# Kernel optimization log

Measured on AMD Instinct MI355X. Metric: run time of the kernel, lower is better.

The kernel has to match this reference:

```python
import jax, jax.numpy as jnp
import numpy as np

N_SRC, N_DST, E = 10000, 40000, 1_280_000
IN_DIM, OUT_DIM, FEAT, O_DIM = 128, 64, 64, 300


def setup_inputs() -> dict:
    key = jax.random.key(0)
    ks = jax.random.split(key, 10)
    s = 0.05
    return {
        "h": jax.random.normal(ks[0], (N_SRC, IN_DIM), jnp.float32),
        "o": jax.random.normal(ks[1], (N_DST, O_DIM), jnp.float32),
        "tfidf": jax.random.normal(ks[2], (E, FEAT), jnp.float32),
        "W_fc": jax.random.normal(ks[3], (IN_DIM, OUT_DIM), jnp.float32) * s,
        "W_fc1": jax.random.normal(ks[4], (O_DIM, OUT_DIM), jnp.float32) * s,
        "W_feat": jax.random.normal(ks[5], (FEAT, OUT_DIM), jnp.float32) * s,
        "b_feat": jax.random.normal(ks[6], (OUT_DIM,), jnp.float32) * s,
        "W_attn": jax.random.normal(ks[7], (OUT_DIM, 1), jnp.float32) * s,
        "edge_src": jax.random.randint(ks[8], (E,), 0, N_SRC, jnp.int32),
        "edge_dst": jax.random.randint(ks[9], (E,), 0, N_DST, jnp.int32),
    }


def reference(h, o, tfidf, W_fc, W_fc1, W_feat, b_feat, W_attn, edge_src, edge_dst):
    n_dst = o.shape[0]
    # node projections: z on sentence (src) nodes via fc, on word (dst) nodes via fc1
    z_src = h @ W_fc                      # [N_SRC, D]
    z_dst = o @ W_fc1                     # [N_DST, D]
    # edge attention: z2 = src.z + dst.z + feat_fc(tfidfembed)
    dfeat = tfidf @ W_feat + b_feat       # [E, D]
    z2 = z_src[edge_src] + z_dst[edge_dst] + dfeat
    z3 = jnp.where(z2 > 0, z2, 0.01 * z2)  # leaky_relu, torch default slope
    e = (z3 @ W_attn)[:, 0]               # [E]
    # segment softmax over incoming edges of each dst (word) node
    m = jax.ops.segment_max(e, edge_dst, num_segments=n_dst)   # [N_DST]
    e_exp = jnp.exp(e - m[edge_dst])                           # [E]
    denom = jax.ops.segment_sum(e_exp, edge_dst, num_segments=n_dst)
    alpha = e_exp / jnp.maximum(denom, 1e-9)[edge_dst]         # [E]
    # weighted sum of src z into dst mailbox
    out = jax.ops.segment_sum(alpha[:, None] * z_src[edge_src], edge_dst,
                              num_segments=n_dst)              # [N_DST, D]
    return out
```

## Files before the change

### kernel.cpp

```cpp
#include <hip/hip_runtime.h>
#include <hip/hip_bf16.h>

#define N_SRC 10000
#define N_DST 40000
#define NE    1280000
#define IN_DIM 128
#define O_DIM  300
#define D      64
#define FEAT   64
#define NB     157

typedef __bf16 bf16x8 __attribute__((ext_vector_type(8)));
typedef __bf16 bf16x4 __attribute__((ext_vector_type(4)));
typedef float  f32x4  __attribute__((ext_vector_type(4)));

__global__ __launch_bounds__(256) void k_zsrc(const float* __restrict__ h,
                                              const float* __restrict__ Wfc,
                                              float* __restrict__ z,
                                              __bf16* __restrict__ zh){
    __shared__ float w[IN_DIM * D];
    for (int i = threadIdx.x; i < IN_DIM * D; i += blockDim.x) w[i] = Wfc[i];
    __syncthreads();
    int lane = threadIdx.x & 63;
    int wid  = blockIdx.x * 4 + (threadIdx.x >> 6);
    int nw   = gridDim.x * 4;
    for (int row = wid; row < N_SRC; row += nw){
        const f32x4* hp = (const f32x4*)(h + (size_t)row * IN_DIM);
        float acc = 0.f;
        #pragma unroll 4
        for (int k4 = 0; k4 < IN_DIM / 4; ++k4){
            f32x4 hv = hp[k4];
            int k = k4 * 4;
            acc += hv[0] * w[(k + 0) * D + lane];
            acc += hv[1] * w[(k + 1) * D + lane];
            acc += hv[2] * w[(k + 2) * D + lane];
            acc += hv[3] * w[(k + 3) * D + lane];
        }
        z[(size_t)row * D + lane]  = acc;
        zh[(size_t)row * D + lane] = (__bf16)acc;
    }
}

__global__ __launch_bounds__(256) void k_zdst(const float* __restrict__ o,
                                              const float* __restrict__ Wfc1,
                                              float* __restrict__ z){
    extern __shared__ float w[];
    for (int i = threadIdx.x; i < O_DIM * D; i += blockDim.x) w[i] = Wfc1[i];
    __syncthreads();
    int lane = threadIdx.x & 63;
    int wid  = blockIdx.x * 4 + (threadIdx.x >> 6);
    int nw   = gridDim.x * 4;
    for (int row = wid; row < N_DST; row += nw){
        const f32x4* op = (const f32x4*)(o + (size_t)row * O_DIM);
        float acc = 0.f;
        #pragma unroll 5
        for (int k4 = 0; k4 < O_DIM / 4; ++k4){
            f32x4 ov = op[k4];
            int k = k4 * 4;
            acc += ov[0] * w[(k + 0) * D + lane];
            acc += ov[1] * w[(k + 1) * D + lane];
            acc += ov[2] * w[(k + 2) * D + lane];
            acc += ov[3] * w[(k + 3) * D + lane];
        }
        z[(size_t)row * D + lane] = acc;
    }
}

__global__ __launch_bounds__(256) void k_hist(const int* __restrict__ edst,
                                              int* __restrict__ cnt){
    int i = blockIdx.x * blockDim.x + threadIdx.x;
    if (i < NE) atomicAdd(&cnt[edst[i]], 1);
}

__device__ __forceinline__ int block_incl_scan(int c, int* wsum){
    int lane = threadIdx.x & 63, w = threadIdx.x >> 6;
    int v = c;
    #pragma unroll
    for (int off = 1; off < 64; off <<= 1){
        int u = __shfl_up(v, off);
        if (lane >= off) v += u;
    }
    if (lane == 63) wsum[w] = v;
    __syncthreads();
    int add = 0;
    for (int ww = 0; ww < w; ++ww) add += wsum[ww];
    return v + add;
}

__global__ __launch_bounds__(256) void k_scan1(const int* __restrict__ cnt,
                                               int* __restrict__ bsum){
    __shared__ int wsum[4];
    int i = blockIdx.x * 256 + threadIdx.x;
    int c = (i < N_DST) ? cnt[i] : 0;
    int lane = threadIdx.x & 63, w = threadIdx.x >> 6;
    int v = c;
    #pragma unroll
    for (int off = 1; off < 64; off <<= 1) v += __shfl_xor(v, off);
    if (lane == 0) wsum[w] = v;
    __syncthreads();
    if (threadIdx.x == 0)
        bsum[blockIdx.x] = wsum[0] + wsum[1] + wsum[2] + wsum[3];
}

__global__ __launch_bounds__(256) void k_scan2(int* __restrict__ bsum){
    __shared__ int wsum[4];
    int i = threadIdx.x;
    int c = (i < NB) ? bsum[i] : 0;
    int v = block_incl_scan(c, wsum);
    if (i < NB) bsum[i] = v - c;
}

__global__ __launch_bounds__(256) void k_scan3(const int* __restrict__ cnt,
                                               const int* __restrict__ bsum,
                                               int* __restrict__ csr,
                                               int* __restrict__ cursor){
    __shared__ int wsum[4];
    int i = blockIdx.x * 256 + threadIdx.x;
    int c = (i < N_DST) ? cnt[i] : 0;
    int v = block_incl_scan(c, wsum);
    int val = bsum[blockIdx.x] + v - c;
    if (i < N_DST){ csr[i] = val; cursor[i] = val; }
    if (blockIdx.x == 0 && threadIdx.x == 0) csr[N_DST] = NE;
}

__global__ __launch_bounds__(256) void k_bucket(const int* __restrict__ esrc,
                                                const int* __restrict__ edst,
                                                int* __restrict__ cursor,
                                                int* __restrict__ ssrc,
                                                int* __restrict__ sdst,
                                                int* __restrict__ sedge){
    int e = blockIdx.x * blockDim.x + threadIdx.x;
    if (e >= NE) return;
    int d = edst[e];
    int pos = atomicAdd(&cursor[d], 1);
    ssrc[pos]  = esrc[e];
    sdst[pos]  = d;
    sedge[pos] = e;
}

__global__ __launch_bounds__(256) void k_edge(
        const float* __restrict__ tfidf,
        const int*   __restrict__ ssrc, const int* __restrict__ sdst,
        const int*   __restrict__ sedge,
        const __bf16* __restrict__ zsrch, const float* __restrict__ zdst,
        const float* __restrict__ Wfeat, const float* __restrict__ bfeat,
        const float* __restrict__ Wattn,
        float* __restrict__ escore_p){
    int lane = threadIdx.x & 63;
    int lo = lane & 15, g = lane >> 4;

    bf16x8 afr[4][2];
    #pragma unroll
    for (int mt = 0; mt < 4; ++mt){
        int m = mt * 16 + lo;
        #pragma unroll
        for (int kh = 0; kh < 2; ++kh){
            #pragma unroll
            for (int j = 0; j < 8; ++j){
                int k = kh * 32 + g * 8 + j;
                afr[mt][kh][j] = (__bf16)Wfeat[k * D + m];
            }
        }
    }
    f32x4 bf4[4], wa4[4];
    #pragma unroll
    for (int mt = 0; mt < 4; ++mt){
        int db = mt * 16 + g * 4;
        bf4[mt] = *(const f32x4*)(bfeat + db);
        wa4[mt] = *(const f32x4*)(Wattn + db);
    }

    int wid = blockIdx.x * 4 + (threadIdx.x >> 6);
    int nw  = gridDim.x * 4;
    for (int tile = wid; tile < NE / 16; tile += nw){
        int p  = tile * 16 + lo;
        int se = sedge[p], ss = ssrc[p], sd = sdst[p];

        const float* trow = tfidf + (size_t)se * FEAT;
        bf16x8 bfr[2];
        #pragma unroll
        for (int kh = 0; kh < 2; ++kh){
            f32x4 fa = *(const f32x4*)(trow + kh * 32 + g * 8);
            f32x4 fb = *(const f32x4*)(trow + kh * 32 + g * 8 + 4);
            #pragma unroll
            for (int j = 0; j < 4; ++j){
                bfr[kh][j]     = (__bf16)fa[j];
                bfr[kh][4 + j] = (__bf16)fb[j];
            }
        }

        float pacc = 0.f;
        #pragma unroll
        for (int mt = 0; mt < 4; ++mt){
            f32x4 acc = {0.f, 0.f, 0.f, 0.f};
            acc = __builtin_amdgcn_mfma_f32_16x16x32_bf16(afr[mt][0], bfr[0], acc, 0, 0, 0);
            acc = __builtin_amdgcn_mfma_f32_16x16x32_bf16(afr[mt][1], bfr[1], acc, 0, 0, 0);
            int db = mt * 16 + g * 4;
            bf16x4 zs = *(const bf16x4*)(zsrch + (size_t)ss * D + db);
            f32x4  zd = *(const f32x4*)(zdst + (size_t)sd * D + db);
            #pragma unroll
            for (int r = 0; r < 4; ++r){
                float z2 = acc[r] + (float)zs[r] + zd[r] + bf4[mt][r];
                float z3 = z2 > 0.f ? z2 : 0.01f * z2;
                pacc += z3 * wa4[mt][r];
            }
        }
        pacc += __shfl_xor(pacc, 16);
        pacc += __shfl_xor(pacc, 32);
        if (lane < 16)
            escore_p[tile * 16 + lane] = pacc;
    }
}

__global__ __launch_bounds__(256) void k_post(const int* __restrict__ csr,
                                              const int* __restrict__ ssrc,
                                              const float* __restrict__ escore_p,
                                              const float* __restrict__ zsrc,
                                              float* __restrict__ out){
    int lane = threadIdx.x & 63;
    int d    = blockIdx.x * 4 + (threadIdx.x >> 6);
    if (d >= N_DST) return;
    int beg = csr[d], end = csr[d + 1];

    float m = -3.4e38f;
    for (int j = beg + lane; j < end; j += 64)
        m = fmaxf(m, escore_p[j]);
    #pragma unroll
    for (int off = 1; off < 64; off <<= 1)
        m = fmaxf(m, __shfl_xor(m, off));

    float ssum = 0.f;
    for (int j = beg + lane; j < end; j += 64)
        ssum += __expf(escore_p[j] - m);
    #pragma unroll
    for (int off = 1; off < 64; off <<= 1)
        ssum += __shfl_xor(ssum, off);
    float inv = 1.f / fmaxf(ssum, 1e-9f);

    float acc = 0.f;
    for (int base = beg; base < end; base += 64){
        int n = end - base; if (n > 64) n = 64;
        int   sj = 0;
        float aj = 0.f;
        if (base + lane < end){
            sj = ssrc[base + lane];
            aj = __expf(escore_p[base + lane] - m) * inv;
        }
        for (int t = 0; t < n; ++t){
            int   s = __shfl(sj, t);
            float a = __shfl(aj, t);
            acc += a * zsrc[(size_t)s * D + lane];
        }
    }
    out[(size_t)d * D + lane] = acc;
}

extern "C" void kernel_launch(void* const* d_in, const int* in_sizes, int n_in,
                              void* d_out, int out_size, void* d_ws, size_t ws_size,
                              hipStream_t stream) {
    const float* h     = (const float*)d_in[0];
    const float* o     = (const float*)d_in[1];
    const float* tfidf = (const float*)d_in[2];
    const float* Wfc   = (const float*)d_in[3];
    const float* Wfc1  = (const float*)d_in[4];
    const float* Wfeat = (const float*)d_in[5];
    const float* bfeat = (const float*)d_in[6];
    const float* Wattn = (const float*)d_in[7];
    const int*   esrc  = (const int*)d_in[8];
    const int*   edst  = (const int*)d_in[9];
    float* out = (float*)d_out;

    float*  ws      = (float*)d_ws;
    float*  zsrc    = ws;
    float*  zdst    = ws + 640000;
    __bf16* zsrch   = (__bf16*)(ws + 3200000);
    float*  escorep = ws + 3520000;
    int*    ssrc    = (int*)(ws + 4800000);
    int*    sdst    = (int*)(ws + 6080000);
    int*    sedge   = (int*)(ws + 7360000);
    int*    cnt     = (int*)(ws + 8640000);
    int*    csr     = (int*)(ws + 8680000);
    int*    cursor  = (int*)(ws + 8720002);
    int*    bsum    = (int*)(ws + 8760002);

    hipMemsetAsync(cnt, 0, N_DST * sizeof(int), stream);

    k_zsrc<<<256, 256, 0, stream>>>(h, Wfc, zsrc, zsrch);
    k_zdst<<<512, 256, O_DIM * D * sizeof(float), stream>>>(o, Wfc1, zdst);
    k_hist<<<NE / 256, 256, 0, stream>>>(edst, cnt);
    k_scan1<<<NB, 256, 0, stream>>>(cnt, bsum);
    k_scan2<<<1, 256, 0, stream>>>(bsum);
    k_scan3<<<NB, 256, 0, stream>>>(cnt, bsum, csr, cursor);
    k_bucket<<<NE / 256, 256, 0, stream>>>(esrc, edst, cursor, ssrc, sdst, sedge);
    k_edge<<<4096, 256, 0, stream>>>(tfidf, ssrc, sdst, sedge, zsrch, zdst,
                                     Wfeat, bfeat, Wattn, escorep);
    k_post<<<N_DST / 4, 256, 0, stream>>>(csr, ssrc, escorep, zsrc, out);
}
```

Measured before the change: 950.3 us.

## Replace bucket pass with atomic ranks and scatter scores from edge kernel

The histogram kernel now records each edge's atomic rank within its destination, and the separate bucket kernel is removed. The edge kernel reads tfidf rows, src and dst in original edge order, so the big tfidf read becomes coalesced instead of a random gather, and it scatters the score and src index to csr[dst]+rank. The projection kernels also compute four rows per wave so each shared-memory weight load is reused across rows. The cost is a scattered write of scores in the edge kernel and a nondeterministic within-segment order from the atomics.

```diff
diff --git a/kernel.cpp b/kernel.cpp
--- a/kernel.cpp
+++ b/kernel.cpp
@@ -24,20 +24,26 @@
     int lane = threadIdx.x & 63;
     int wid  = blockIdx.x * 4 + (threadIdx.x >> 6);
     int nw   = gridDim.x * 4;
-    for (int row = wid; row < N_SRC; row += nw){
-        const f32x4* hp = (const f32x4*)(h + (size_t)row * IN_DIM);
-        float acc = 0.f;
+    for (int r0 = wid * 4; r0 < N_SRC; r0 += nw * 4){
+        const f32x4* p0 = (const f32x4*)(h + (size_t)(r0 + 0) * IN_DIM);
+        const f32x4* p1 = (const f32x4*)(h + (size_t)(r0 + 1) * IN_DIM);
+        const f32x4* p2 = (const f32x4*)(h + (size_t)(r0 + 2) * IN_DIM);
+        const f32x4* p3 = (const f32x4*)(h + (size_t)(r0 + 3) * IN_DIM);
+        float a0 = 0.f, a1 = 0.f, a2 = 0.f, a3 = 0.f;
         #pragma unroll 4
         for (int k4 = 0; k4 < IN_DIM / 4; ++k4){
-            f32x4 hv = hp[k4];
-            int k = k4 * 4;
-            acc += hv[0] * w[(k + 0) * D + lane];
-            acc += hv[1] * w[(k + 1) * D + lane];
-            acc += hv[2] * w[(k + 2) * D + lane];
-            acc += hv[3] * w[(k + 3) * D + lane];
-        }
-        z[(size_t)row * D + lane]  = acc;
-        zh[(size_t)row * D + lane] = (__bf16)acc;
+            f32x4 v0 = p0[k4], v1 = p1[k4], v2 = p2[k4], v3 = p3[k4];
+            #pragma unroll
+            for (int i = 0; i < 4; ++i){
+                float wv = w[(k4 * 4 + i) * D + lane];
+                a0 += v0[i] * wv; a1 += v1[i] * wv;
+                a2 += v2[i] * wv; a3 += v3[i] * wv;
+            }
+        }
+        z[(size_t)(r0 + 0) * D + lane] = a0; zh[(size_t)(r0 + 0) * D + lane] = (__bf16)a0;
+        z[(size_t)(r0 + 1) * D + lane] = a1; zh[(size_t)(r0 + 1) * D + lane] = (__bf16)a1;
+        z[(size_t)(r0 + 2) * D + lane] = a2; zh[(size_t)(r0 + 2) * D + lane] = (__bf16)a2;
+        z[(size_t)(r0 + 3) * D + lane] = a3; zh[(size_t)(r0 + 3) * D + lane] = (__bf16)a3;
     }
 }
 
@@ -50,26 +56,34 @@
     int lane = threadIdx.x & 63;
     int wid  = blockIdx.x * 4 + (threadIdx.x >> 6);
     int nw   = gridDim.x * 4;
-    for (int row = wid; row < N_DST; row += nw){
-        const f32x4* op = (const f32x4*)(o + (size_t)row * O_DIM);
-        float acc = 0.f;
+    for (int r0 = wid * 4; r0 < N_DST; r0 += nw * 4){
+        const f32x4* p0 = (const f32x4*)(o + (size_t)(r0 + 0) * O_DIM);
+        const f32x4* p1 = (const f32x4*)(o + (size_t)(r0 + 1) * O_DIM);
+        const f32x4* p2 = (const f32x4*)(o + (size_t)(r0 + 2) * O_DIM);
+        const f32x4* p3 = (const f32x4*)(o + (size_t)(r0 + 3) * O_DIM);
+        float a0 = 0.f, a1 = 0.f, a2 = 0.f, a3 = 0.f;
         #pragma unroll 5
         for (int k4 = 0; k4 < O_DIM / 4; ++k4){
-            f32x4 ov = op[k4];
-            int k = k4 * 4;
-            acc += ov[0] * w[(k + 0) * D + lane];
-            acc += ov[1] * w[(k + 1) * D + lane];
-            acc += ov[2] * w[(k + 2) * D + lane];
-            acc += ov[3] * w[(k + 3) * D + lane];
-        }
-        z[(size_t)row * D + lane] = acc;
-    }
-}
-
-__global__ __launch_bounds__(256) void k_hist(const int* __restrict__ edst,
-                                              int* __restrict__ cnt){
+            f32x4 v0 = p0[k4], v1 = p1[k4], v2 = p2[k4], v3 = p3[k4];
+            #pragma unroll
+            for (int i = 0; i < 4; ++i){
+                float wv = w[(k4 * 4 + i) * D + lane];
+                a0 += v0[i] * wv; a1 += v1[i] * wv;
+                a2 += v2[i] * wv; a3 += v3[i] * wv;
+            }
+        }
+        z[(size_t)(r0 + 0) * D + lane] = a0;
+        z[(size_t)(r0 + 1) * D + lane] = a1;
+        z[(size_t)(r0 + 2) * D + lane] = a2;
+        z[(size_t)(r0 + 3) * D + lane] = a3;
+    }
+}
+
+__global__ __launch_bounds__(256) void k_rank(const int* __restrict__ edst,
+                                              int* __restrict__ cnt,
+                                              int* __restrict__ rank){
     int i = blockIdx.x * blockDim.x + threadIdx.x;
-    if (i < NE) atomicAdd(&cnt[edst[i]], 1);
+    if (i < NE) rank[i] = atomicAdd(&cnt[edst[i]], 1);
 }
 
 __device__ __forceinline__ int block_incl_scan(int c, int* wsum){
@@ -112,40 +126,24 @@
 
 __global__ __launch_bounds__(256) void k_scan3(const int* __restrict__ cnt,
                                                const int* __restrict__ bsum,
-                                               int* __restrict__ csr,
-                                               int* __restrict__ cursor){
+                                               int* __restrict__ csr){
     __shared__ int wsum[4];
     int i = blockIdx.x * 256 + threadIdx.x;
     int c = (i < N_DST) ? cnt[i] : 0;
     int v = block_incl_scan(c, wsum);
     int val = bsum[blockIdx.x] + v - c;
-    if (i < N_DST){ csr[i] = val; cursor[i] = val; }
+    if (i < N_DST) csr[i] = val;
     if (blockIdx.x == 0 && threadIdx.x == 0) csr[N_DST] = NE;
-}
-
-__global__ __launch_bounds__(256) void k_bucket(const int* __restrict__ esrc,
-                                                const int* __restrict__ edst,
-                                                int* __restrict__ cursor,
-                                                int* __restrict__ ssrc,
-                                                int* __restrict__ sdst,
-                                                int* __restrict__ sedge){
-    int e = blockIdx.x * blockDim.x + threadIdx.x;
-    if (e >= NE) return;
-    int d = edst[e];
-    int pos = atomicAdd(&cursor[d], 1);
-    ssrc[pos]  = esrc[e];
-    sdst[pos]  = d;
-    sedge[pos] = e;
 }
 
 __global__ __launch_bounds__(256) void k_edge(
         const float* __restrict__ tfidf,
-        const int*   __restrict__ ssrc, const int* __restrict__ sdst,
-        const int*   __restrict__ sedge,
+        const int*   __restrict__ esrc, const int* __restrict__ edst,
+        const int*   __restrict__ rank, const int* __restrict__ csr,
         const __bf16* __restrict__ zsrch, const float* __restrict__ zdst,
         const float* __restrict__ Wfeat, const float* __restrict__ bfeat,
         const float* __restrict__ Wattn,
-        float* __restrict__ escore_p){
+        float* __restrict__ escore_p, int* __restrict__ ssrc_s){
     int lane = threadIdx.x & 63;
     int lo = lane & 15, g = lane >> 4;
 
@@ -173,10 +171,12 @@
     int wid = blockIdx.x * 4 + (threadIdx.x >> 6);
     int nw  = gridDim.x * 4;
     for (int tile = wid; tile < NE / 16; tile += nw){
-        int p  = tile * 16 + lo;
-        int se = sedge[p], ss = ssrc[p], sd = sdst[p];
-
-        const float* trow = tfidf + (size_t)se * FEAT;
+        int e  = tile * 16 + lo;
+        int ss = esrc[e];
+        int sd = edst[e];
+        int rk = rank[e];
+
+        const float* trow = tfidf + (size_t)e * FEAT;
         bf16x8 bfr[2];
         #pragma unroll
         for (int kh = 0; kh < 2; ++kh){
@@ -207,8 +207,11 @@
         }
         pacc += __shfl_xor(pacc, 16);
         pacc += __shfl_xor(pacc, 32);
-        if (lane < 16)
-            escore_p[tile * 16 + lane] = pacc;
+        if (lane < 16){
+            int pos = csr[sd] + rk;
+            escore_p[pos] = pacc;
+            ssrc_s[pos]   = ss;
+        }
     }
 }
 
@@ -276,23 +279,20 @@
     __bf16* zsrch   = (__bf16*)(ws + 3200000);
     float*  escorep = ws + 3520000;
     int*    ssrc    = (int*)(ws + 4800000);
-    int*    sdst    = (int*)(ws + 6080000);
-    int*    sedge   = (int*)(ws + 7360000);
-    int*    cnt     = (int*)(ws + 8640000);
-    int*    csr     = (int*)(ws + 8680000);
-    int*    cursor  = (int*)(ws + 8720002);
-    int*    bsum    = (int*)(ws + 8760002);
+    int*    rank    = (int*)(ws + 6080000);
+    int*    cnt     = (int*)(ws + 7360000);
+    int*    csr     = (int*)(ws + 7400000);
+    int*    bsum    = (int*)(ws + 7440002);
 
     hipMemsetAsync(cnt, 0, N_DST * sizeof(int), stream);
 
     k_zsrc<<<256, 256, 0, stream>>>(h, Wfc, zsrc, zsrch);
     k_zdst<<<512, 256, O_DIM * D * sizeof(float), stream>>>(o, Wfc1, zdst);
-    k_hist<<<NE / 256, 256, 0, stream>>>(edst, cnt);
+    k_rank<<<NE / 256, 256, 0, stream>>>(edst, cnt, rank);
     k_scan1<<<NB, 256, 0, stream>>>(cnt, bsum);
     k_scan2<<<1, 256, 0, stream>>>(bsum);
-    k_scan3<<<NB, 256, 0, stream>>>(cnt, bsum, csr, cursor);
-    k_bucket<<<NE / 256, 256, 0, stream>>>(esrc, edst, cursor, ssrc, sdst, sedge);
-    k_edge<<<4096, 256, 0, stream>>>(tfidf, ssrc, sdst, sedge, zsrch, zdst,
-                                     Wfeat, bfeat, Wattn, escorep);
+    k_scan3<<<NB, 256, 0, stream>>>(cnt, bsum, csr);
+    k_edge<<<4096, 256, 0, stream>>>(tfidf, esrc, edst, rank, csr, zsrch, zdst,
+                                     Wfeat, bfeat, Wattn, escorep, ssrc);
     k_post<<<N_DST / 4, 256, 0, stream>>>(csr, ssrc, escorep, zsrc, out);
 }
```

After: 857.3 us. -9.8%, faster.
